# Kernel optimization log

Measured on AMD Instinct MI355X. Metric: run time of the kernel, lower is better.

The kernel has to match this reference:

```python
import jax, jax.numpy as jnp
import numpy as np

DIM = 1024
N_HEADS = 16
HEAD_DIM = DIM // N_HEADS
B, T = 2, 2048


def setup_inputs() -> dict:
    key = jax.random.key(0)
    ks = jax.random.split(key, 5)
    x = jax.random.normal(ks[0], (B, T, DIM), dtype=jnp.float32)
    s = DIM ** -0.5
    Wq = jax.random.normal(ks[1], (DIM, DIM), dtype=jnp.float32) * s
    Wk = jax.random.normal(ks[2], (DIM, DIM), dtype=jnp.float32) * s
    Wv = jax.random.normal(ks[3], (DIM, DIM), dtype=jnp.float32) * s
    Wo = jax.random.normal(ks[4], (DIM, DIM), dtype=jnp.float32) * s
    # causal mask: 1 where attendable, 0 where masked (masked_fill on mask==0)
    mask = jnp.tril(jnp.ones((T, T), dtype=jnp.int32))[None, None, :, :]
    return {"x": x, "Wq": Wq, "Wk": Wk, "Wv": Wv, "Wo": Wo, "mask": mask}


def _rope_tables(seq_len, dim, dtype):
    inv_freq = 1.0 / (10000.0 ** (jnp.arange(0, dim, 2, dtype=jnp.float32) / dim))
    t = jnp.arange(seq_len, dtype=jnp.float32)
    freqs = jnp.outer(t, inv_freq)               # [T, dim/2]
    emb = jnp.concatenate([freqs, freqs], -1)    # [T, dim]
    return jnp.cos(emb).astype(dtype), jnp.sin(emb).astype(dtype)


def _rotate_half(t):
    h = t.shape[-1] // 2
    return jnp.concatenate([-t[..., h:], t[..., :h]], axis=-1)


def reference(x, Wq, Wk, Wv, Wo, mask):
    Bq, Tq, C = x.shape
    H, Dh = N_HEADS, C // N_HEADS
    q = (x @ Wq.T).reshape(Bq, Tq, H, Dh)
    k = (x @ Wk.T).reshape(Bq, Tq, H, Dh)
    v = (x @ Wv.T).reshape(Bq, Tq, H, Dh)
    cos, sin = _rope_tables(Tq, Dh, x.dtype)
    cos = cos[None, :, None, :]   # [1,T,1,Dh]
    sin = sin[None, :, None, :]
    q = q * cos + _rotate_half(q) * sin
    k = k * cos + _rotate_half(k) * sin
    scale = Dh ** -0.5
    # [B,H,T,T]
    attn = jnp.einsum('bqhd,bkhd->bhqk', q, k) * scale
    attn = jnp.where(mask == 0, jnp.float32(-jnp.inf).astype(attn.dtype), attn)
    attn = jax.nn.softmax(attn, axis=-1)
    out = jnp.einsum('bhqk,bkhd->bqhd', attn, v).reshape(Bq, Tq, C)
    return out @ Wo.T
```

## Files before the change

kernel.cpp:

```cpp
#include <hip/hip_runtime.h>
#include <stdint.h>


typedef float  f32x4  __attribute__((ext_vector_type(4)));
typedef __bf16 bf16x8 __attribute__((ext_vector_type(8)));
typedef __bf16 bf16x4 __attribute__((ext_vector_type(4)));

#define GLDS16(gp, lp)                                                         \
  __builtin_amdgcn_global_load_lds(                                            \
      (const __attribute__((address_space(1))) void*)(gp),                     \
      (__attribute__((address_space(3))) void*)(lp), 16, 0, 0)

static __device__ __forceinline__ f32x4 zero4() {
  f32x4 z = {0.f, 0.f, 0.f, 0.f};
  return z;
}

static __device__ __forceinline__ bf16x8 cvt8(const float* __restrict__ p) {
  f32x4 u = *(const f32x4*)p;
  f32x4 v = *(const f32x4*)(p + 4);
  bf16x8 o;
#pragma unroll
  for (int j = 0; j < 4; ++j) o[j] = (__bf16)u[j];
#pragma unroll
  for (int j = 0; j < 4; ++j) o[4 + j] = (__bf16)v[j];
  return o;
}

__global__ __launch_bounds__(256) void prep(
    const float* __restrict__ x,
    const float* __restrict__ Wq, const float* __restrict__ Wk,
    const float* __restrict__ Wv, const float* __restrict__ Wo,
    __bf16* __restrict__ xb, __bf16* __restrict__ Wb)
{
  size_t g = ((size_t)blockIdx.x * 256 + threadIdx.x) * 8;
  if (g < (size_t)4194304) {
    *(bf16x8*)&xb[g] = cvt8(x + g);
  } else {
    size_t j = g - 4194304;
    int w = (int)(j >> 20);
    size_t off = j & 1048575;
    const float* src = (w == 0) ? Wq : (w == 1) ? Wk : (w == 2) ? Wv : Wo;
    *(bf16x8*)&Wb[(size_t)w * 1048576 + off] = cvt8(src + off);
  }
}

__global__ __launch_bounds__(256) void gemm_qkv(
    const __bf16* __restrict__ xb, const __bf16* __restrict__ Wb,
    __bf16* __restrict__ Qp, __bf16* __restrict__ Kp, __bf16* __restrict__ Vt)
{
  __shared__ __bf16 As[128 * 32];
  __shared__ __bf16 Bs[128 * 32];
  __shared__ __bf16 Es[4 * 16 * 72];

  const int tid  = threadIdx.x;
  const int lane = tid & 63;
  const int wid  = tid >> 6;
  const int quad = lane >> 4;
  const int l16  = lane & 15;
  const int wm   = (wid >> 1) * 64;
  const int wn   = (wid & 1) * 64;

  const int lin = blockIdx.x;
  const int n0  = (lin & 7) * 128;
  const int r2  = lin >> 3;
  const int z   = r2 % 3;
  const int m0  = (r2 / 3) * 128;
  const __bf16* Bt = Wb + (size_t)z * 1048576;

  const int r0 = tid >> 2, c0 = tid & 3;
  const int r1 = (tid + 256) >> 2;

  f32x4 acc[4][4];
  for (int i = 0; i < 4; ++i)
    for (int j = 0; j < 4; ++j) acc[i][j] = zero4();

  for (int k0 = 0; k0 < 1024; k0 += 32) {
    __syncthreads();
    GLDS16(xb + (size_t)(m0 + r0) * 1024 + k0 + c0 * 8, &As[(size_t)tid * 8]);
    GLDS16(xb + (size_t)(m0 + r1) * 1024 + k0 + c0 * 8, &As[(size_t)(tid + 256) * 8]);
    GLDS16(Bt + (size_t)(n0 + r0) * 1024 + k0 + c0 * 8, &Bs[(size_t)tid * 8]);
    GLDS16(Bt + (size_t)(n0 + r1) * 1024 + k0 + c0 * 8, &Bs[(size_t)(tid + 256) * 8]);
    __syncthreads();

    bf16x8 af[4], bfr[4];
    for (int i = 0; i < 4; ++i)
      af[i] = *(const bf16x8*)&As[(wm + i * 16 + l16) * 32 + quad * 8];
    for (int i = 0; i < 4; ++i)
      bfr[i] = *(const bf16x8*)&Bs[(wn + i * 16 + l16) * 32 + quad * 8];
    for (int mt = 0; mt < 4; ++mt)
      for (int nt = 0; nt < 4; ++nt)
        acc[mt][nt] = __builtin_amdgcn_mfma_f32_16x16x32_bf16(
            af[mt], bfr[nt], acc[mt][nt], 0, 0, 0);
  }

  const int h = (n0 + wn) >> 6;
  __bf16* es = &Es[wid * 1152];
  const int rl = lane >> 3, ch = lane & 7;

  if (z < 2) {
    const float c0f = -13.287712379549449f / 32.0f;
    const float f0 = exp2f((float)l16 * c0f);
    const float f1 = exp2f((float)(16 + l16) * c0f);
    const float SC = (z == 0) ? 0.125f * 1.44269504088896340736f : 1.0f;
    for (int mt = 0; mt < 4; ++mt)
      for (int r = 0; r < 4; ++r) {
        int gm = m0 + wm + mt * 16 + 4 * quad + r;
        float t = (float)(gm & 2047);
        for (int nt = 0; nt < 2; ++nt) {
          float ang = t * (nt ? f1 : f0);
          float cv = __cosf(ang) * SC, sv = __sinf(ang) * SC;
          float lo = acc[mt][nt][r], hi = acc[mt][nt + 2][r];
          acc[mt][nt][r]     = lo * cv - hi * sv;
          acc[mt][nt + 2][r] = hi * cv + lo * sv;
        }
      }
    __bf16* dst = (z == 0) ? Qp : Kp;
    for (int mt = 0; mt < 4; ++mt) {
      for (int nt = 0; nt < 4; ++nt)
        for (int r = 0; r < 4; ++r)
          es[(4 * quad + r) * 72 + nt * 16 + l16] = (__bf16)acc[mt][nt][r];
      size_t g0 = (size_t)(m0 + wm + mt * 16 + rl) * 1024 + n0 + wn + ch * 8;
      *(bf16x8*)&dst[g0]            = *(const bf16x8*)&es[rl * 72 + ch * 8];
      *(bf16x8*)&dst[g0 + 8 * 1024] = *(const bf16x8*)&es[(rl + 8) * 72 + ch * 8];
    }
  } else {
    const int b = m0 >> 11;
    const size_t hb = (size_t)(b * 16 + h) * 64;
    const int tt = (m0 + wm) & 2047;
    for (int nt = 0; nt < 4; ++nt) {
      for (int mt = 0; mt < 4; ++mt)
        for (int r = 0; r < 4; ++r)
          es[l16 * 72 + mt * 16 + 4 * quad + r] = (__bf16)acc[mt][nt][r];
      size_t g0 = (hb + nt * 16 + rl) * 2048 + tt + ch * 8;
      *(bf16x8*)&Vt[g0]                     = *(const bf16x8*)&es[rl * 72 + ch * 8];
      *(bf16x8*)&Vt[g0 + (size_t)8 * 2048]  = *(const bf16x8*)&es[(rl + 8) * 72 + ch * 8];
    }
  }
}

__global__ __launch_bounds__(256) void attn_fwd(
    __bf16* QA, const __bf16* __restrict__ Kp,
    const __bf16* __restrict__ Vt)
{
  __shared__ __bf16 Ks[2][64 * 72];
  __shared__ __bf16 Vs[2][64 * 72];
  __shared__ __bf16 Ps[64 * 72];

  const int tid  = threadIdx.x;
  const int lane = tid & 63, wid = tid >> 6;
  const int quad = lane >> 4, l16 = lane & 15;

  const int L  = blockIdx.x;
  const int j  = L >> 3;
  const int qb = 31 - (j >> 2);
  const int bh = (L & 7) * 4 + (j & 3);
  const int b = bh >> 4, h = bh & 15;
  const int q0 = qb * 64;

  const size_t rowb = (size_t)b * 2048;
  const __bf16* Vb = Vt + (size_t)bh * 64 * 2048;

  const int sr0 = tid >> 3, sc0 = tid & 7;
  const int sr1 = (tid + 256) >> 3;
  const int iq = wid * 16 + l16;

  bf16x8 qa[2];
  for (int ks = 0; ks < 2; ++ks)
    qa[ks] = *(const bf16x8*)
        &QA[(rowb + q0 + iq) * 1024 + h * 64 + ks * 32 + quad * 8];

  f32x4 oacc[4];
  for (int i = 0; i < 4; ++i) oacc[i] = zero4();
  float l_i = 0.f;

  const f32x4 minit = {-16.f, -16.f, -16.f, -16.f};

  const int kcmax = qb;

  bf16x8 k0v, k1v, v0v, v1v;
  k0v = *(const bf16x8*)&Kp[(rowb + sr0) * 1024 + h * 64 + sc0 * 8];
  k1v = *(const bf16x8*)&Kp[(rowb + sr1) * 1024 + h * 64 + sc0 * 8];
  v0v = *(const bf16x8*)&Vb[(size_t)sr0 * 2048 + sc0 * 8];
  v1v = *(const bf16x8*)&Vb[(size_t)sr1 * 2048 + sc0 * 8];
  *(bf16x8*)&Ks[0][sr0 * 72 + sc0 * 8] = k0v;
  *(bf16x8*)&Ks[0][sr1 * 72 + sc0 * 8] = k1v;
  *(bf16x8*)&Vs[0][sr0 * 72 + sc0 * 8] = v0v;
  *(bf16x8*)&Vs[0][sr1 * 72 + sc0 * 8] = v1v;
  if (kcmax > 0) {
    k0v = *(const bf16x8*)&Kp[(rowb + 64 + sr0) * 1024 + h * 64 + sc0 * 8];
    k1v = *(const bf16x8*)&Kp[(rowb + 64 + sr1) * 1024 + h * 64 + sc0 * 8];
    v0v = *(const bf16x8*)&Vb[(size_t)sr0 * 2048 + 64 + sc0 * 8];
    v1v = *(const bf16x8*)&Vb[(size_t)sr1 * 2048 + 64 + sc0 * 8];
  }
  __syncthreads();

  for (int kc = 0; kc <= kcmax; ++kc) {
    const int c = kc & 1;
    if (kc < kcmax) {
      *(bf16x8*)&Ks[c ^ 1][sr0 * 72 + sc0 * 8] = k0v;
      *(bf16x8*)&Ks[c ^ 1][sr1 * 72 + sc0 * 8] = k1v;
      *(bf16x8*)&Vs[c ^ 1][sr0 * 72 + sc0 * 8] = v0v;
      *(bf16x8*)&Vs[c ^ 1][sr1 * 72 + sc0 * 8] = v1v;
    }
    if (kc + 2 <= kcmax) {
      const int kn = kc + 2;
      k0v = *(const bf16x8*)&Kp[(rowb + kn * 64 + sr0) * 1024 + h * 64 + sc0 * 8];
      k1v = *(const bf16x8*)&Kp[(rowb + kn * 64 + sr1) * 1024 + h * 64 + sc0 * 8];
      v0v = *(const bf16x8*)&Vb[(size_t)sr0 * 2048 + kn * 64 + sc0 * 8];
      v1v = *(const bf16x8*)&Vb[(size_t)sr1 * 2048 + kn * 64 + sc0 * 8];
    }

    f32x4 sacc[4];
    for (int i = 0; i < 4; ++i) sacc[i] = minit;
    __builtin_amdgcn_s_setprio(1);
    for (int ks = 0; ks < 2; ++ks) {
      bf16x8 qf = qa[ks];
      for (int mt = 0; mt < 4; ++mt) {
        bf16x8 kf = *(const bf16x8*)
            &Ks[c][(mt * 16 + l16) * 72 + ks * 32 + quad * 8];
        sacc[mt] = __builtin_amdgcn_mfma_f32_16x16x32_bf16(
            kf, qf, sacc[mt], 0, 0, 0);
      }
    }
    __builtin_amdgcn_s_setprio(0);

    const bool diag = (kc == kcmax);
    float rsum = 0.f;
    for (int mt = 0; mt < 4; ++mt) {
      bf16x4 pw;
      for (int r = 0; r < 4; ++r) {
        float s = sacc[mt][r];
        if (diag && (mt * 16 + 4 * quad + r > iq)) s = -1e30f;
        float p = __builtin_amdgcn_exp2f(s);
        rsum += p;
        pw[r] = (__bf16)p;
      }
      *(bf16x4*)&Ps[iq * 72 + mt * 16 + 4 * quad] = pw;
    }
    rsum += __shfl_xor(rsum, 16, 64);
    rsum += __shfl_xor(rsum, 32, 64);
    l_i += rsum;

    __builtin_amdgcn_s_setprio(1);
    for (int ks = 0; ks < 2; ++ks) {
      bf16x8 pf = *(const bf16x8*)
          &Ps[(wid * 16 + l16) * 72 + ks * 32 + quad * 8];
      for (int nt = 0; nt < 4; ++nt) {
        bf16x8 vf = *(const bf16x8*)
            &Vs[c][(nt * 16 + l16) * 72 + ks * 32 + quad * 8];
        oacc[nt] = __builtin_amdgcn_mfma_f32_16x16x32_bf16(
            pf, vf, oacc[nt], 0, 0, 0);
      }
    }
    __builtin_amdgcn_s_setprio(0);

    __syncthreads();
  }

  {
    float invl = 1.0f / l_i;
    for (int r = 0; r < 4; ++r) {
      float inv_r = __shfl(invl, 4 * quad + r, 64);
      for (int nt = 0; nt < 4; ++nt)
        Ps[(wid * 16 + 4 * quad + r) * 72 + nt * 16 + l16] =
            (__bf16)(oacc[nt][r] * inv_r);
    }
  }
  __syncthreads();
  {
    int row = tid >> 3, ch = tid & 7;
    size_t g0 = (rowb + q0 + row) * 1024 + h * 64 + ch * 8;
    *(bf16x8*)&QA[g0]                   = *(const bf16x8*)&Ps[row * 72 + ch * 8];
    *(bf16x8*)&QA[g0 + (size_t)32 * 1024] =
        *(const bf16x8*)&Ps[(row + 32) * 72 + ch * 8];
  }
}

__global__ __launch_bounds__(256) void gemm_out(
    const __bf16* __restrict__ AO, const __bf16* __restrict__ Wob,
    float* __restrict__ Of)
{
  __shared__ __bf16 As[128 * 32];
  __shared__ __bf16 Bs[128 * 32];
  __shared__ float  EsF[4 * 16 * 68];

  const int tid  = threadIdx.x;
  const int lane = tid & 63;
  const int wid  = tid >> 6;
  const int quad = lane >> 4;
  const int l16  = lane & 15;
  const int wm   = (wid >> 1) * 64;
  const int wn   = (wid & 1) * 64;
  const int lin = blockIdx.x;
  const int n0  = (lin & 7) * 128;
  const int m0  = (lin >> 3) * 128;

  const int r0 = tid >> 2, c0 = tid & 3;
  const int r1 = (tid + 256) >> 2;

  f32x4 acc[4][4];
  for (int i = 0; i < 4; ++i)
    for (int j = 0; j < 4; ++j) acc[i][j] = zero4();

  for (int k0 = 0; k0 < 1024; k0 += 32) {
    __syncthreads();
    GLDS16(AO  + (size_t)(m0 + r0) * 1024 + k0 + c0 * 8, &As[(size_t)tid * 8]);
    GLDS16(AO  + (size_t)(m0 + r1) * 1024 + k0 + c0 * 8, &As[(size_t)(tid + 256) * 8]);
    GLDS16(Wob + (size_t)(n0 + r0) * 1024 + k0 + c0 * 8, &Bs[(size_t)tid * 8]);
    GLDS16(Wob + (size_t)(n0 + r1) * 1024 + k0 + c0 * 8, &Bs[(size_t)(tid + 256) * 8]);
    __syncthreads();

    bf16x8 af[4], bfr[4];
    for (int i = 0; i < 4; ++i)
      af[i] = *(const bf16x8*)&As[(wm + i * 16 + l16) * 32 + quad * 8];
    for (int i = 0; i < 4; ++i)
      bfr[i] = *(const bf16x8*)&Bs[(wn + i * 16 + l16) * 32 + quad * 8];
    for (int mt = 0; mt < 4; ++mt)
      for (int nt = 0; nt < 4; ++nt)
        acc[mt][nt] = __builtin_amdgcn_mfma_f32_16x16x32_bf16(
            af[mt], bfr[nt], acc[mt][nt], 0, 0, 0);
  }

  float* es = &EsF[wid * 1088];
  const int rl = lane >> 4, ch = lane & 15;
  for (int mt = 0; mt < 4; ++mt) {
    for (int nt = 0; nt < 4; ++nt)
      for (int r = 0; r < 4; ++r)
        es[(4 * quad + r) * 68 + nt * 16 + l16] = acc[mt][nt][r];
    size_t g0 = (size_t)(m0 + wm + mt * 16 + rl) * 1024 + n0 + wn + ch * 4;
    *(f32x4*)&Of[g0]             = *(const f32x4*)&es[rl * 68 + ch * 4];
    *(f32x4*)&Of[g0 + 4 * 1024]  = *(const f32x4*)&es[(rl + 4) * 68 + ch * 4];
    *(f32x4*)&Of[g0 + 8 * 1024]  = *(const f32x4*)&es[(rl + 8) * 68 + ch * 4];
    *(f32x4*)&Of[g0 + 12 * 1024] = *(const f32x4*)&es[(rl + 12) * 68 + ch * 4];
  }
}

__global__ __launch_bounds__(256) void copy_bf16x8(
    const __bf16* __restrict__ src, __bf16* __restrict__ dst)
{
  size_t i = ((size_t)blockIdx.x * 256 + threadIdx.x) * 8;
  *(bf16x8*)&dst[i] = *(const bf16x8*)&src[i];
}

extern "C" void kernel_launch(void* const* d_in, const int* in_sizes, int n_in,
                              void* d_out, int out_size, void* d_ws, size_t ws_size,
                              hipStream_t stream) {
  const float* x  = (const float*)d_in[0];
  const float* Wq = (const float*)d_in[1];
  const float* Wk = (const float*)d_in[2];
  const float* Wv = (const float*)d_in[3];
  const float* Wo = (const float*)d_in[4];
  float* out = (float*)d_out;

  const size_t NELT = (size_t)4194304;
  __bf16* Qp = (__bf16*)d_ws;
  __bf16* Kp = Qp + NELT;
  __bf16* Vt = Kp + NELT;
  __bf16* xb = (__bf16*)d_out;
  __bf16* Wb = xb + NELT;

  prep<<<dim3(4096), 256, 0, stream>>>(x, Wq, Wk, Wv, Wo, xb, Wb);
  gemm_qkv<<<dim3(768), 256, 0, stream>>>(xb, Wb, Qp, Kp, Vt);
  attn_fwd<<<dim3(1024), 256, 0, stream>>>(Qp, Kp, Vt);
  copy_bf16x8<<<dim3(512), 256, 0, stream>>>(Wb + 3 * NELT / 4, Kp);
  gemm_out<<<dim3(256), 256, 0, stream>>>(Qp, Kp, out);
}
```

Before: 196.2 us.

## Restructure attention to 32x32 MFMA with register-resident P and split-K waves

The attention kernel switches from 16x16x32 to 32x32x16 bf16 MFMA tiles. Each wave now owns a 32-query by 32-key quadrant, and the P matrix stays in registers via cvt_pk and permlane32_swap instead of going through an LDS round trip. K/V tiles are loaded with direct global-to-LDS loads into an XOR-swizzled unpadded layout, replacing the register-staged prefetch. The two key-half waves reduce their partial outputs and row sums through LDS at the end. The aim is to cut LDS traffic and barrier cost, but it adds a cross-wave reduction and gives only one tile of prefetch depth.

```diff
diff --git a/kernel.cpp b/kernel.cpp
--- a/kernel.cpp
+++ b/kernel.cpp
@@ -3,8 +3,9 @@
 
 
 typedef float  f32x4  __attribute__((ext_vector_type(4)));
+typedef float  f32x16 __attribute__((ext_vector_type(16)));
 typedef __bf16 bf16x8 __attribute__((ext_vector_type(8)));
-typedef __bf16 bf16x4 __attribute__((ext_vector_type(4)));
+typedef unsigned int u32x2 __attribute__((ext_vector_type(2)));
 
 #define GLDS16(gp, lp)                                                         \
   __builtin_amdgcn_global_load_lds(                                            \
@@ -143,13 +144,13 @@
     __bf16* QA, const __bf16* __restrict__ Kp,
     const __bf16* __restrict__ Vt)
 {
-  __shared__ __bf16 Ks[2][64 * 72];
-  __shared__ __bf16 Vs[2][64 * 72];
-  __shared__ __bf16 Ps[64 * 72];
+  __shared__ __bf16 Ks[2][64 * 64];
+  __shared__ __bf16 Vs[2][64 * 64];
 
   const int tid  = threadIdx.x;
   const int lane = tid & 63, wid = tid >> 6;
-  const int quad = lane >> 4, l16 = lane & 15;
+  const int hl = lane >> 5, lq = lane & 31, lq7 = lq & 7;
+  const int qh = wid & 1, kh = wid >> 1;
 
   const int L  = blockIdx.x;
   const int j  = L >> 3;
@@ -161,119 +162,150 @@
   const size_t rowb = (size_t)b * 2048;
   const __bf16* Vb = Vt + (size_t)bh * 64 * 2048;
 
-  const int sr0 = tid >> 3, sc0 = tid & 7;
-  const int sr1 = (tid + 256) >> 3;
-  const int iq = wid * 16 + l16;
-
-  bf16x8 qa[2];
-  for (int ks = 0; ks < 2; ++ks)
+  const int srow = lane >> 3;
+  const int scol = ((lane & 7) ^ srow) * 8;
+  const int ck0 = wid * 2, ck1 = wid * 2 + 1;
+
+  const int iql = qh * 32 + lq;
+
+  bf16x8 qa[4];
+#pragma unroll
+  for (int ks = 0; ks < 4; ++ks)
     qa[ks] = *(const bf16x8*)
-        &QA[(rowb + q0 + iq) * 1024 + h * 64 + ks * 32 + quad * 8];
-
-  f32x4 oacc[4];
-  for (int i = 0; i < 4; ++i) oacc[i] = zero4();
+        &QA[(rowb + q0 + iql) * 1024 + h * 64 + ks * 16 + hl * 8];
+
+  f32x16 oacc[2];
+#pragma unroll
+  for (int dt = 0; dt < 2; ++dt)
+#pragma unroll
+    for (int r = 0; r < 16; ++r) oacc[dt][r] = 0.f;
   float l_i = 0.f;
 
-  const f32x4 minit = {-16.f, -16.f, -16.f, -16.f};
-
   const int kcmax = qb;
 
-  bf16x8 k0v, k1v, v0v, v1v;
-  k0v = *(const bf16x8*)&Kp[(rowb + sr0) * 1024 + h * 64 + sc0 * 8];
-  k1v = *(const bf16x8*)&Kp[(rowb + sr1) * 1024 + h * 64 + sc0 * 8];
-  v0v = *(const bf16x8*)&Vb[(size_t)sr0 * 2048 + sc0 * 8];
-  v1v = *(const bf16x8*)&Vb[(size_t)sr1 * 2048 + sc0 * 8];
-  *(bf16x8*)&Ks[0][sr0 * 72 + sc0 * 8] = k0v;
-  *(bf16x8*)&Ks[0][sr1 * 72 + sc0 * 8] = k1v;
-  *(bf16x8*)&Vs[0][sr0 * 72 + sc0 * 8] = v0v;
-  *(bf16x8*)&Vs[0][sr1 * 72 + sc0 * 8] = v1v;
-  if (kcmax > 0) {
-    k0v = *(const bf16x8*)&Kp[(rowb + 64 + sr0) * 1024 + h * 64 + sc0 * 8];
-    k1v = *(const bf16x8*)&Kp[(rowb + 64 + sr1) * 1024 + h * 64 + sc0 * 8];
-    v0v = *(const bf16x8*)&Vb[(size_t)sr0 * 2048 + 64 + sc0 * 8];
-    v1v = *(const bf16x8*)&Vb[(size_t)sr1 * 2048 + 64 + sc0 * 8];
-  }
+  GLDS16(Kp + (rowb + ck0 * 8 + srow) * 1024 + h * 64 + scol, &Ks[0][ck0 * 512]);
+  GLDS16(Kp + (rowb + ck1 * 8 + srow) * 1024 + h * 64 + scol, &Ks[0][ck1 * 512]);
+  GLDS16(Vb + (size_t)(ck0 * 8 + srow) * 2048 + scol, &Vs[0][ck0 * 512]);
+  GLDS16(Vb + (size_t)(ck1 * 8 + srow) * 2048 + scol, &Vs[0][ck1 * 512]);
   __syncthreads();
 
   for (int kc = 0; kc <= kcmax; ++kc) {
     const int c = kc & 1;
     if (kc < kcmax) {
-      *(bf16x8*)&Ks[c ^ 1][sr0 * 72 + sc0 * 8] = k0v;
-      *(bf16x8*)&Ks[c ^ 1][sr1 * 72 + sc0 * 8] = k1v;
-      *(bf16x8*)&Vs[c ^ 1][sr0 * 72 + sc0 * 8] = v0v;
-      *(bf16x8*)&Vs[c ^ 1][sr1 * 72 + sc0 * 8] = v1v;
-    }
-    if (kc + 2 <= kcmax) {
-      const int kn = kc + 2;
-      k0v = *(const bf16x8*)&Kp[(rowb + kn * 64 + sr0) * 1024 + h * 64 + sc0 * 8];
-      k1v = *(const bf16x8*)&Kp[(rowb + kn * 64 + sr1) * 1024 + h * 64 + sc0 * 8];
-      v0v = *(const bf16x8*)&Vb[(size_t)sr0 * 2048 + kn * 64 + sc0 * 8];
-      v1v = *(const bf16x8*)&Vb[(size_t)sr1 * 2048 + kn * 64 + sc0 * 8];
-    }
-
-    f32x4 sacc[4];
-    for (int i = 0; i < 4; ++i) sacc[i] = minit;
+      const int t0 = (kc + 1) * 64;
+      GLDS16(Kp + (rowb + t0 + ck0 * 8 + srow) * 1024 + h * 64 + scol,
+             &Ks[c ^ 1][ck0 * 512]);
+      GLDS16(Kp + (rowb + t0 + ck1 * 8 + srow) * 1024 + h * 64 + scol,
+             &Ks[c ^ 1][ck1 * 512]);
+      GLDS16(Vb + (size_t)(ck0 * 8 + srow) * 2048 + t0 + scol,
+             &Vs[c ^ 1][ck0 * 512]);
+      GLDS16(Vb + (size_t)(ck1 * 8 + srow) * 2048 + t0 + scol,
+             &Vs[c ^ 1][ck1 * 512]);
+    }
+
+    const __bf16* Ksb = Ks[c];
+    const __bf16* Vsb = Vs[c];
+
+    f32x16 sacc;
+#pragma unroll
+    for (int r = 0; r < 16; ++r) sacc[r] = -16.f;
     __builtin_amdgcn_s_setprio(1);
-    for (int ks = 0; ks < 2; ++ks) {
-      bf16x8 qf = qa[ks];
-      for (int mt = 0; mt < 4; ++mt) {
-        bf16x8 kf = *(const bf16x8*)
-            &Ks[c][(mt * 16 + l16) * 72 + ks * 32 + quad * 8];
-        sacc[mt] = __builtin_amdgcn_mfma_f32_16x16x32_bf16(
-            kf, qf, sacc[mt], 0, 0, 0);
-      }
+#pragma unroll
+    for (int ks = 0; ks < 4; ++ks) {
+      bf16x8 kf = *(const bf16x8*)
+          &Ksb[(kh * 32 + lq) * 64 + (((2 * ks + hl) ^ lq7) * 8)];
+      sacc = __builtin_amdgcn_mfma_f32_32x32x16_bf16(kf, qa[ks], sacc, 0, 0, 0);
     }
     __builtin_amdgcn_s_setprio(0);
 
     const bool diag = (kc == kcmax);
+    float p[16];
     float rsum = 0.f;
-    for (int mt = 0; mt < 4; ++mt) {
-      bf16x4 pw;
-      for (int r = 0; r < 4; ++r) {
-        float s = sacc[mt][r];
-        if (diag && (mt * 16 + 4 * quad + r > iq)) s = -1e30f;
-        float p = __builtin_amdgcn_exp2f(s);
-        rsum += p;
-        pw[r] = (__bf16)p;
-      }
-      *(bf16x4*)&Ps[iq * 72 + mt * 16 + 4 * quad] = pw;
-    }
-    rsum += __shfl_xor(rsum, 16, 64);
+#pragma unroll
+    for (int r = 0; r < 16; ++r) {
+      float s = sacc[r];
+      if (diag) {
+        int kp = kh * 32 + (r & 3) + 8 * (r >> 2) + 4 * hl;
+        if (kp > iql) s = -1e30f;
+      }
+      p[r] = __builtin_amdgcn_exp2f(s);
+      rsum += p[r];
+    }
     rsum += __shfl_xor(rsum, 32, 64);
     l_i += rsum;
 
+    unsigned int cpk[8];
+#pragma unroll
+    for (int i = 0; i < 8; ++i)
+      asm("v_cvt_pk_bf16_f32 %0, %1, %2"
+          : "=v"(cpk[i]) : "v"(p[2 * i]), "v"(p[2 * i + 1]));
+    bf16x8 pb[2];
+#pragma unroll
+    for (int k2 = 0; k2 < 2; ++k2) {
+      unsigned int a0 = cpk[4 * k2 + 0], b0 = cpk[4 * k2 + 2];
+      unsigned int a1 = cpk[4 * k2 + 1], b1 = cpk[4 * k2 + 3];
+      asm("v_permlane32_swap_b32 %0, %1" : "+v"(a0), "+v"(b0));
+      asm("v_permlane32_swap_b32 %0, %1" : "+v"(a1), "+v"(b1));
+      union { unsigned int w[4]; bf16x8 v; } u;
+      u.w[0] = a0; u.w[1] = a1; u.w[2] = b0; u.w[3] = b1;
+      pb[k2] = u.v;
+    }
+
     __builtin_amdgcn_s_setprio(1);
-    for (int ks = 0; ks < 2; ++ks) {
-      bf16x8 pf = *(const bf16x8*)
-          &Ps[(wid * 16 + l16) * 72 + ks * 32 + quad * 8];
-      for (int nt = 0; nt < 4; ++nt) {
+#pragma unroll
+    for (int dt = 0; dt < 2; ++dt)
+#pragma unroll
+      for (int k2 = 0; k2 < 2; ++k2) {
         bf16x8 vf = *(const bf16x8*)
-            &Vs[c][(nt * 16 + l16) * 72 + ks * 32 + quad * 8];
-        oacc[nt] = __builtin_amdgcn_mfma_f32_16x16x32_bf16(
-            pf, vf, oacc[nt], 0, 0, 0);
-      }
-    }
+            &Vsb[(dt * 32 + lq) * 64 + (((4 * kh + 2 * k2 + hl) ^ lq7) * 8)];
+        oacc[dt] = __builtin_amdgcn_mfma_f32_32x32x16_bf16(
+            vf, pb[k2], oacc[dt], 0, 0, 0);
+      }
     __builtin_amdgcn_s_setprio(0);
 
     __syncthreads();
   }
 
-  {
-    float invl = 1.0f / l_i;
-    for (int r = 0; r < 4; ++r) {
-      float inv_r = __shfl(invl, 4 * quad + r, 64);
-      for (int nt = 0; nt < 4; ++nt)
-        Ps[(wid * 16 + 4 * quad + r) * 72 + nt * 16 + l16] =
-            (__bf16)(oacc[nt][r] * inv_r);
-    }
+  float* Osf = (float*)&Ks[0][0];
+  float* Lsf = (float*)&Vs[0][0];
+  if (kh == 1) {
+#pragma unroll
+    for (int dt = 0; dt < 2; ++dt) {
+      float* base = &Osf[((qh * 2 + dt) * 64 + lane) * 16];
+#pragma unroll
+      for (int g = 0; g < 4; ++g) {
+        f32x4 w = {oacc[dt][4 * g], oacc[dt][4 * g + 1],
+                   oacc[dt][4 * g + 2], oacc[dt][4 * g + 3]};
+        *(f32x4*)&base[4 * g] = w;
+      }
+    }
+    Lsf[qh * 64 + lane] = l_i;
   }
   __syncthreads();
-  {
-    int row = tid >> 3, ch = tid & 7;
-    size_t g0 = (rowb + q0 + row) * 1024 + h * 64 + ch * 8;
-    *(bf16x8*)&QA[g0]                   = *(const bf16x8*)&Ps[row * 72 + ch * 8];
-    *(bf16x8*)&QA[g0 + (size_t)32 * 1024] =
-        *(const bf16x8*)&Ps[(row + 32) * 72 + ch * 8];
+  if (kh == 0) {
+#pragma unroll
+    for (int dt = 0; dt < 2; ++dt) {
+      const float* base = &Osf[((qh * 2 + dt) * 64 + lane) * 16];
+#pragma unroll
+      for (int g = 0; g < 4; ++g) {
+        f32x4 w = *(const f32x4*)&base[4 * g];
+#pragma unroll
+        for (int e = 0; e < 4; ++e) oacc[dt][4 * g + e] += w[e];
+      }
+    }
+    float inv = 1.0f / (l_i + Lsf[qh * 64 + lane]);
+#pragma unroll
+    for (int dt = 0; dt < 2; ++dt)
+#pragma unroll
+      for (int g = 0; g < 4; ++g) {
+        float a = oacc[dt][4 * g]     * inv, bb = oacc[dt][4 * g + 1] * inv;
+        float cc = oacc[dt][4 * g + 2] * inv, dd = oacc[dt][4 * g + 3] * inv;
+        unsigned int w0, w1;
+        asm("v_cvt_pk_bf16_f32 %0, %1, %2" : "=v"(w0) : "v"(a), "v"(bb));
+        asm("v_cvt_pk_bf16_f32 %0, %1, %2" : "=v"(w1) : "v"(cc), "v"(dd));
+        u32x2 wv = {w0, w1};
+        *(u32x2*)&QA[(rowb + q0 + iql) * 1024 + h * 64 + dt * 32 + 8 * g + 4 * hl] = wv;
+      }
   }
 }
 
```

New measurement: 193.9 us. No clear change (-1.1%).
